# Optimization experiments

Measured on AMD Instinct MI355X. Metric: run time of the kernel, lower is better.

## Reference

```python
import jax, jax.numpy as jnp
import numpy as np

N_NODES = 100000
N_EDGES = 3200000  # avg degree 32
EPS = 1e-12


def setup_inputs() -> dict:
    key = jax.random.key(0)
    k1, k2, k3, k4, k5 = jax.random.split(key, 5)
    positions = jax.random.normal(k1, (N_NODES, 3), dtype=jnp.float32)
    node_feat = jnp.ones((N_NODES, 1), dtype=jnp.float32)  # dummy 1x0e data
    w0 = jax.random.normal(k2, (1,), dtype=jnp.float32)    # linear weight for 0e output
    w1 = jax.random.normal(k3, (3,), dtype=jnp.float32)    # linear weight for 1o output (elementwise)
    edge_src = jax.random.randint(k4, (N_EDGES,), 0, N_NODES, dtype=jnp.int32)
    edge_dst = jax.random.randint(k5, (N_EDGES,), 0, N_NODES, dtype=jnp.int32)
    return {"positions": positions, "node_feat": node_feat, "w0": w0, "w1": w1,
            "edge_src": edge_src, "edge_dst": edge_dst}


def reference(positions, node_feat, w0, w1, edge_src, edge_dst):
    n_nodes = positions.shape[0]
    # relative positions per edge: dest - src  [E,3]
    rel = positions[edge_dst] - positions[edge_src]
    # spherical harmonics lmax=1: Y0 = 1 (constant 0e), Y1 = unit direction (1o)
    norm = jnp.sqrt(jnp.sum(rel * rel, axis=-1, keepdims=True))
    sh1 = rel / jnp.maximum(norm, EPS)                      # [E,3]
    # gather dest-node scalar feature (code gathers dest_node_feat)
    s = node_feat[edge_dst]                                 # [E,1]
    # tensor product of 0e scalar with (0e + 1o): tp0 = s*1, tp1 = s*sh1
    # LinearLayer: elementwise multiply by per-irrep weight vectors
    out0 = w0 * s                                           # [E,1]
    out1 = w1 * (s * sh1)                                   # [E,3]
    edge_out = jnp.concatenate([out0, out1], axis=-1)       # [E,4]
    # scatter-mean aggregation over incoming edges per dest node
    sums = jax.ops.segment_sum(edge_out, edge_dst, num_segments=n_nodes)
    ones = jnp.ones((edge_out.shape[0], 1), dtype=edge_out.dtype)
    counts = jax.ops.segment_sum(ones, edge_dst, num_segments=n_nodes)
    return sums / jnp.maximum(counts, 1.0)                  # [N,4]
```

## Files before the change

### kernel.cpp

```cpp
#include <hip/hip_runtime.h>


#define EPS 1e-12f
#define FSCALE 128.0f
#define FBIAS 128
#define CHUNK_SHIFT 12
#define CHUNK 4096
#define NCHUNK_MAX 32
#define BLKA 512
#define TPA 4
#define NSTAGE (BLKA * TPA)
#define BLKB 512
#define SUBS 12
#define SHARDS 16

__global__ void repack_pos(const float* __restrict__ pos,
                           float4* __restrict__ pos4, int n_nodes) {
    int n = blockIdx.x * blockDim.x + threadIdx.x;
    if (n >= n_nodes) return;
    float4 p;
    p.x = pos[3 * n + 0];
    p.y = pos[3 * n + 1];
    p.z = pos[3 * n + 2];
    p.w = 0.f;
    pos4[n] = p;
}

__global__ __launch_bounds__(BLKA) void phaseA(
        const float4* __restrict__ pos4,
        const int* __restrict__ dst,
        const int* __restrict__ src,
        unsigned* __restrict__ gcnt,
        unsigned long long* __restrict__ recs,
        int n_edges, int capx, int n_chunk) {
    __shared__ unsigned long long stage[NSTAGE];
    __shared__ unsigned h[NCHUNK_MAX];
    __shared__ unsigned pref[NCHUNK_MAX + 1];
    __shared__ unsigned gbase[NCHUNK_MAX];
    int tid = threadIdx.x;
    int shard = (int)blockIdx.x & (SHARDS - 1);
    if (tid < n_chunk) h[tid] = 0;
    __syncthreads();

    long e0 = (long)blockIdx.x * NSTAGE;
    unsigned long long rec[TPA];
    int ch[TPA];
    unsigned rank[TPA];
    bool val[TPA];
#pragma unroll
    for (int t = 0; t < TPA; ++t) {
        long j = e0 + (long)t * BLKA + tid;
        val[t] = (j < n_edges);
        if (val[t]) {
            int d = dst[j];
            int s = src[j];
            float4 pd = pos4[d];
            float4 ps = pos4[s];
            float rx = pd.x - ps.x;
            float ry = pd.y - ps.y;
            float rz = pd.z - ps.z;
            float inv = 1.0f / fmaxf(sqrtf(rx * rx + ry * ry + rz * rz), EPS);
            unsigned fx = (unsigned)(FBIAS + (int)rintf(rx * inv * FSCALE));
            unsigned fy = (unsigned)(FBIAS + (int)rintf(ry * inv * FSCALE));
            unsigned fz = (unsigned)(FBIAS + (int)rintf(rz * inv * FSCALE));
            unsigned local = (unsigned)d & (CHUNK - 1);
            ch[t] = d >> CHUNK_SHIFT;
            rec[t] = ((unsigned long long)local << 27)
                   | ((unsigned long long)fx << 18)
                   | ((unsigned long long)fy << 9)
                   | (unsigned long long)fz;
            rank[t] = atomicAdd(&h[ch[t]], 1u);
        }
    }
    __syncthreads();
    if (tid == 0) {
        unsigned run = 0;
        for (int c = 0; c < n_chunk; ++c) { pref[c] = run; run += h[c]; }
        pref[n_chunk] = run;
    }
    if (tid < n_chunk)
        gbase[tid] = h[tid] ? atomicAdd(&gcnt[shard * NCHUNK_MAX + tid], h[tid]) : 0u;
    __syncthreads();
#pragma unroll
    for (int t = 0; t < TPA; ++t)
        if (val[t]) stage[pref[ch[t]] + rank[t]] = rec[t];
    __syncthreads();
    unsigned total = pref[n_chunk];
    for (unsigned i = tid; i < total; i += BLKA) {
        int lo = 0, hi = n_chunk - 1;
        while (lo < hi) {
            int mid = (lo + hi + 1) >> 1;
            if (pref[mid] <= i) lo = mid; else hi = mid - 1;
        }
        unsigned idx = gbase[lo] + (i - pref[lo]);
        if (idx < (unsigned)capx)
            recs[(size_t)(shard * n_chunk + lo) * (unsigned)capx + idx] = stage[i];
    }
}

__global__ __launch_bounds__(BLKB) void phaseB(
        const unsigned* __restrict__ gcnt,
        const unsigned long long* __restrict__ recs,
        unsigned long long* __restrict__ accR,
        int capx, int n_chunk, int padded) {
    __shared__ unsigned long long lds[CHUNK];
    int c   = (int)blockIdx.x % n_chunk;
    int sub = (int)blockIdx.x / n_chunk;

    for (int i = threadIdx.x; i < CHUNK; i += BLKB) lds[i] = 0ull;
    __syncthreads();

    for (int s16 = 0; s16 < SHARDS; ++s16) {
        unsigned cnt = gcnt[s16 * NCHUNK_MAX + c];
        if (cnt > (unsigned)capx) cnt = (unsigned)capx;
        const unsigned long long* bucket =
            recs + (size_t)(s16 * n_chunk + c) * (unsigned)capx;
        for (unsigned j = (unsigned)sub * BLKB + threadIdx.x; j < cnt;
             j += (unsigned)SUBS * BLKB) {
            unsigned long long r = bucket[j];
            unsigned local = (unsigned)(r >> 27);
            unsigned long long p = (((r >> 18) & 511ull) << 48)
                                 | (((r >>  9) & 511ull) << 32)
                                 | (((r      ) & 511ull) << 16)
                                 | 1ull;
            atomicAdd(&lds[local], p);
        }
    }
    __syncthreads();

    unsigned long long* row = accR + (size_t)sub * (unsigned)padded
                                   + (size_t)c * CHUNK;
    for (int i = threadIdx.x; i < CHUNK; i += BLKB) row[i] = lds[i];
}

__global__ void finalize_binned(const unsigned long long* __restrict__ accR,
                                const float* __restrict__ feat,
                                const float* __restrict__ w0,
                                const float* __restrict__ w1,
                                float* __restrict__ out,
                                int n_nodes, int padded) {
    int n = blockIdx.x * blockDim.x + threadIdx.x;
    if (n >= n_nodes) return;
    int Fx = 0, Fy = 0, Fz = 0, C = 0;
    for (int s = 0; s < SUBS; ++s) {
        unsigned long long v = accR[(size_t)s * (unsigned)padded + (unsigned)n];
        Fx += (int)(v >> 48);
        Fy += (int)((v >> 32) & 0xffffull);
        Fz += (int)((v >> 16) & 0xffffull);
        C  += (int)(v & 0xffffull);
    }
    float c = (float)C;
    float rd = 1.0f / fmaxf(c, 1.0f);
    float sx = (float)Fx * (1.0f / FSCALE) - c;
    float sy = (float)Fy * (1.0f / FSCALE) - c;
    float sz = (float)Fz * (1.0f / FSCALE) - c;
    float f = feat[n];
    float4 o;
    o.x = w0[0] * f * c * rd;
    o.y = w1[0] * f * sx * rd;
    o.z = w1[1] * f * sy * rd;
    o.w = w1[2] * f * sz * rd;
    ((float4*)out)[n] = o;
}

__global__ void edge_kernel_agent(const float* __restrict__ pos,
                                  const int* __restrict__ dst,
                                  const int* __restrict__ src,
                                  unsigned long long* __restrict__ acc,
                                  int n_edges, int n_nodes, int rmask) {
    int i = blockIdx.x * blockDim.x + threadIdx.x;
    if (i >= n_edges) return;
    int s = src[i];
    int d = dst[i];
    float rx = pos[3 * d + 0] - pos[3 * s + 0];
    float ry = pos[3 * d + 1] - pos[3 * s + 1];
    float rz = pos[3 * d + 2] - pos[3 * s + 2];
    float nrm = sqrtf(rx * rx + ry * ry + rz * rz);
    float inv = 1.0f / fmaxf(nrm, EPS);
    unsigned fx = (unsigned)(FBIAS + (int)rintf(rx * inv * FSCALE));
    unsigned fy = (unsigned)(FBIAS + (int)rintf(ry * inv * FSCALE));
    unsigned fz = (unsigned)(FBIAS + (int)rintf(rz * inv * FSCALE));
    unsigned long long p = ((unsigned long long)fx << 48)
                         | ((unsigned long long)fy << 32)
                         | ((unsigned long long)fz << 16) | 1ull;
    unsigned r = (unsigned)blockIdx.x & (unsigned)rmask;
    atomicAdd(acc + (size_t)r * (unsigned)n_nodes + (unsigned)d, p);
}

__global__ void finalize_flat(const unsigned long long* __restrict__ acc,
                              const float* __restrict__ feat,
                              const float* __restrict__ w0,
                              const float* __restrict__ w1,
                              float* __restrict__ out,
                              int n_nodes, int R) {
    int n = blockIdx.x * blockDim.x + threadIdx.x;
    if (n >= n_nodes) return;
    int Fx = 0, Fy = 0, Fz = 0, C = 0;
    for (int r = 0; r < R; ++r) {
        unsigned long long v = acc[(size_t)r * n_nodes + n];
        Fx += (int)(v >> 48);
        Fy += (int)((v >> 32) & 0xffffull);
        Fz += (int)((v >> 16) & 0xffffull);
        C  += (int)(v & 0xffffull);
    }
    float c = (float)C;
    float rd = 1.0f / fmaxf(c, 1.0f);
    float sx = (float)Fx * (1.0f / FSCALE) - c;
    float sy = (float)Fy * (1.0f / FSCALE) - c;
    float sz = (float)Fz * (1.0f / FSCALE) - c;
    float f = feat[n];
    float4 o;
    o.x = w0[0] * f * c * rd;
    o.y = w1[0] * f * sx * rd;
    o.z = w1[1] * f * sy * rd;
    o.w = w1[2] * f * sz * rd;
    ((float4*)out)[n] = o;
}

extern "C" void kernel_launch(void* const* d_in, const int* in_sizes, int n_in,
                              void* d_out, int out_size, void* d_ws, size_t ws_size,
                              hipStream_t stream) {
    const float* pos  = (const float*)d_in[0];
    const float* feat = (const float*)d_in[1];
    const float* w0   = (const float*)d_in[2];
    const float* w1   = (const float*)d_in[3];
    const int* esrc   = (const int*)d_in[4];
    const int* edst   = (const int*)d_in[5];
    int n_nodes = in_sizes[0] / 3;
    int n_edges = in_sizes[4];

    int n_chunk = (n_nodes + CHUNK - 1) >> CHUNK_SHIFT;
    int padded  = n_chunk * CHUNK;
    int capx = (int)((long)n_edges / ((long)SHARDS * n_chunk) + 4096);

    size_t off_pos4 = 0;
    size_t pos4_bytes = (size_t)padded * sizeof(float4);
    size_t off_gcnt = (pos4_bytes + 255) & ~(size_t)255;
    size_t gcnt_bytes = (size_t)SHARDS * NCHUNK_MAX * sizeof(unsigned);
    size_t off_recs = off_gcnt + ((gcnt_bytes + 255) & ~(size_t)255);
    size_t recs_bytes = (size_t)SHARDS * n_chunk * (unsigned)capx
                      * sizeof(unsigned long long);
    size_t off_accR = off_recs + ((recs_bytes + 255) & ~(size_t)255);
    size_t accR_bytes = (size_t)SUBS * (unsigned)padded * sizeof(unsigned long long);
    size_t need = off_accR + accR_bytes;

    int nb = 256;
    int ng = (n_nodes + nb - 1) / nb;

    if (n_chunk <= NCHUNK_MAX && ws_size >= need) {
        float4* pos4 = (float4*)((char*)d_ws + off_pos4);
        unsigned* gcnt = (unsigned*)((char*)d_ws + off_gcnt);
        unsigned long long* recs = (unsigned long long*)((char*)d_ws + off_recs);
        unsigned long long* accR = (unsigned long long*)((char*)d_ws + off_accR);

        hipMemsetAsync(gcnt, 0, gcnt_bytes, stream);
        repack_pos<<<ng, nb, 0, stream>>>(pos, pos4, n_nodes);

        int ga = (int)((n_edges + (long)NSTAGE - 1) / (long)NSTAGE);
        phaseA<<<ga, BLKA, 0, stream>>>(pos4, edst, esrc, gcnt, recs,
                                        n_edges, capx, n_chunk);
        phaseB<<<n_chunk * SUBS, BLKB, 0, stream>>>(gcnt, recs, accR,
                                                    capx, n_chunk, padded);
        finalize_binned<<<ng, nb, 0, stream>>>(accR, feat, w0, w1,
                                               (float*)d_out, n_nodes, padded);
    } else {
        int R = 4;
        while (R > 1 && (size_t)R * n_nodes * sizeof(unsigned long long) > ws_size) R >>= 1;
        unsigned long long* acc = (unsigned long long*)d_ws;
        hipMemsetAsync(acc, 0, (size_t)R * n_nodes * sizeof(unsigned long long), stream);
        int eb = 256;
        int eg = (n_edges + eb - 1) / eb;
        edge_kernel_agent<<<eg, eb, 0, stream>>>(pos, edst, esrc, acc,
                                                 n_edges, n_nodes, R - 1);
        finalize_flat<<<ng, nb, 0, stream>>>(acc, feat, w0, w1,
                                             (float*)d_out, n_nodes, R);
    }
}
```

Before: 133.2 us.

## Move geometry compute to phase B and bin compact 32-bit edge records

After: 119.8 us. 10.0% less time.

```diff
diff --git a/kernel.cpp b/kernel.cpp
--- a/kernel.cpp
+++ b/kernel.cpp
@@ -4,36 +4,38 @@
 #define EPS 1e-12f
 #define FSCALE 128.0f
 #define FBIAS 128
-#define CHUNK_SHIFT 12
-#define CHUNK 4096
-#define NCHUNK_MAX 32
+#define CHUNK_SHIFT 11
+#define CHUNK 2048
+#define NCHUNK_MAX 64
 #define BLKA 512
 #define TPA 4
 #define NSTAGE (BLKA * TPA)
 #define BLKB 512
-#define SUBS 12
 #define SHARDS 16
 
 __global__ void repack_pos(const float* __restrict__ pos,
-                           float4* __restrict__ pos4, int n_nodes) {
+                           float4* __restrict__ pos4,
+                           unsigned* __restrict__ gcnt,
+                           int n_nodes, int padded) {
     int n = blockIdx.x * blockDim.x + threadIdx.x;
-    if (n >= n_nodes) return;
-    float4 p;
-    p.x = pos[3 * n + 0];
-    p.y = pos[3 * n + 1];
-    p.z = pos[3 * n + 2];
-    p.w = 0.f;
+    if (n < SHARDS * NCHUNK_MAX) gcnt[n] = 0;
+    if (n >= padded) return;
+    float4 p = make_float4(0.f, 0.f, 0.f, 0.f);
+    if (n < n_nodes) {
+        p.x = pos[3 * n + 0];
+        p.y = pos[3 * n + 1];
+        p.z = pos[3 * n + 2];
+    }
     pos4[n] = p;
 }
 
 __global__ __launch_bounds__(BLKA) void phaseA(
-        const float4* __restrict__ pos4,
         const int* __restrict__ dst,
         const int* __restrict__ src,
         unsigned* __restrict__ gcnt,
-        unsigned long long* __restrict__ recs,
+        unsigned* __restrict__ recs,
         int n_edges, int capx, int n_chunk) {
-    __shared__ unsigned long long stage[NSTAGE];
+    __shared__ unsigned stage[NSTAGE];
     __shared__ unsigned h[NCHUNK_MAX];
     __shared__ unsigned pref[NCHUNK_MAX + 1];
     __shared__ unsigned gbase[NCHUNK_MAX];
@@ -43,7 +45,7 @@
     __syncthreads();
 
     long e0 = (long)blockIdx.x * NSTAGE;
-    unsigned long long rec[TPA];
+    unsigned rec[TPA];
     int ch[TPA];
     unsigned rank[TPA];
     bool val[TPA];
@@ -54,21 +56,8 @@
         if (val[t]) {
             int d = dst[j];
             int s = src[j];
-            float4 pd = pos4[d];
-            float4 ps = pos4[s];
-            float rx = pd.x - ps.x;
-            float ry = pd.y - ps.y;
-            float rz = pd.z - ps.z;
-            float inv = 1.0f / fmaxf(sqrtf(rx * rx + ry * ry + rz * rz), EPS);
-            unsigned fx = (unsigned)(FBIAS + (int)rintf(rx * inv * FSCALE));
-            unsigned fy = (unsigned)(FBIAS + (int)rintf(ry * inv * FSCALE));
-            unsigned fz = (unsigned)(FBIAS + (int)rintf(rz * inv * FSCALE));
-            unsigned local = (unsigned)d & (CHUNK - 1);
             ch[t] = d >> CHUNK_SHIFT;
-            rec[t] = ((unsigned long long)local << 27)
-                   | ((unsigned long long)fx << 18)
-                   | ((unsigned long long)fy << 9)
-                   | (unsigned long long)fz;
+            rec[t] = ((unsigned)(d & (CHUNK - 1)) << 17) | (unsigned)s;
             rank[t] = atomicAdd(&h[ch[t]], 1u);
         }
     }
@@ -100,37 +89,47 @@
 
 __global__ __launch_bounds__(BLKB) void phaseB(
         const unsigned* __restrict__ gcnt,
-        const unsigned long long* __restrict__ recs,
+        const unsigned* __restrict__ recs,
+        const float4* __restrict__ pos4,
         unsigned long long* __restrict__ accR,
         int capx, int n_chunk, int padded) {
-    __shared__ unsigned long long lds[CHUNK];
-    int c   = (int)blockIdx.x % n_chunk;
-    int sub = (int)blockIdx.x / n_chunk;
-
-    for (int i = threadIdx.x; i < CHUNK; i += BLKB) lds[i] = 0ull;
-    __syncthreads();
-
-    for (int s16 = 0; s16 < SHARDS; ++s16) {
-        unsigned cnt = gcnt[s16 * NCHUNK_MAX + c];
-        if (cnt > (unsigned)capx) cnt = (unsigned)capx;
-        const unsigned long long* bucket =
-            recs + (size_t)(s16 * n_chunk + c) * (unsigned)capx;
-        for (unsigned j = (unsigned)sub * BLKB + threadIdx.x; j < cnt;
-             j += (unsigned)SUBS * BLKB) {
-            unsigned long long r = bucket[j];
-            unsigned local = (unsigned)(r >> 27);
-            unsigned long long p = (((r >> 18) & 511ull) << 48)
-                                 | (((r >>  9) & 511ull) << 32)
-                                 | (((r      ) & 511ull) << 16)
-                                 | 1ull;
-            atomicAdd(&lds[local], p);
-        }
-    }
-    __syncthreads();
-
-    unsigned long long* row = accR + (size_t)sub * (unsigned)padded
-                                   + (size_t)c * CHUNK;
-    for (int i = threadIdx.x; i < CHUNK; i += BLKB) row[i] = lds[i];
+    __shared__ unsigned long long acc[CHUNK];
+    __shared__ float4 posw[CHUNK];
+    int c     = (int)blockIdx.x % n_chunk;
+    int shard = (int)blockIdx.x / n_chunk;
+    int base  = c << CHUNK_SHIFT;
+
+    for (int i = threadIdx.x; i < CHUNK; i += BLKB) {
+        acc[i] = 0ull;
+        posw[i] = pos4[base + i];
+    }
+    __syncthreads();
+
+    unsigned cnt = gcnt[shard * NCHUNK_MAX + c];
+    if (cnt > (unsigned)capx) cnt = (unsigned)capx;
+    const unsigned* bucket = recs + (size_t)(shard * n_chunk + c) * (unsigned)capx;
+    for (unsigned j = threadIdx.x; j < cnt; j += BLKB) {
+        unsigned r = bucket[j];
+        unsigned s = r & 0x1FFFFu;
+        unsigned local = r >> 17;
+        float4 ps = pos4[s];
+        float4 pd = posw[local];
+        float rx = pd.x - ps.x;
+        float ry = pd.y - ps.y;
+        float rz = pd.z - ps.z;
+        float inv = 1.0f / fmaxf(sqrtf(rx * rx + ry * ry + rz * rz), EPS);
+        unsigned fx = (unsigned)(FBIAS + (int)rintf(rx * inv * FSCALE));
+        unsigned fy = (unsigned)(FBIAS + (int)rintf(ry * inv * FSCALE));
+        unsigned fz = (unsigned)(FBIAS + (int)rintf(rz * inv * FSCALE));
+        unsigned long long p = ((unsigned long long)fx << 48)
+                             | ((unsigned long long)fy << 32)
+                             | ((unsigned long long)fz << 16) | 1ull;
+        atomicAdd(&acc[local], p);
+    }
+    __syncthreads();
+
+    unsigned long long* row = accR + (size_t)shard * (unsigned)padded + base;
+    for (int i = threadIdx.x; i < CHUNK; i += BLKB) row[i] = acc[i];
 }
 
 __global__ void finalize_binned(const unsigned long long* __restrict__ accR,
@@ -142,7 +141,7 @@
     int n = blockIdx.x * blockDim.x + threadIdx.x;
     if (n >= n_nodes) return;
     int Fx = 0, Fy = 0, Fz = 0, C = 0;
-    for (int s = 0; s < SUBS; ++s) {
+    for (int s = 0; s < SHARDS; ++s) {
         unsigned long long v = accR[(size_t)s * (unsigned)padded + (unsigned)n];
         Fx += (int)(v >> 48);
         Fy += (int)((v >> 32) & 0xffffull);
@@ -175,8 +174,7 @@
     float rx = pos[3 * d + 0] - pos[3 * s + 0];
     float ry = pos[3 * d + 1] - pos[3 * s + 1];
     float rz = pos[3 * d + 2] - pos[3 * s + 2];
-    float nrm = sqrtf(rx * rx + ry * ry + rz * rz);
-    float inv = 1.0f / fmaxf(nrm, EPS);
+    float inv = 1.0f / fmaxf(sqrtf(rx * rx + ry * ry + rz * rz), EPS);
     unsigned fx = (unsigned)(FBIAS + (int)rintf(rx * inv * FSCALE));
     unsigned fy = (unsigned)(FBIAS + (int)rintf(ry * inv * FSCALE));
     unsigned fz = (unsigned)(FBIAS + (int)rintf(rz * inv * FSCALE));
@@ -231,36 +229,35 @@
 
     int n_chunk = (n_nodes + CHUNK - 1) >> CHUNK_SHIFT;
     int padded  = n_chunk * CHUNK;
-    int capx = (int)((long)n_edges / ((long)SHARDS * n_chunk) + 4096);
+    int capx = (int)((long)n_edges / ((long)SHARDS * n_chunk) + 1024);
 
     size_t off_pos4 = 0;
     size_t pos4_bytes = (size_t)padded * sizeof(float4);
     size_t off_gcnt = (pos4_bytes + 255) & ~(size_t)255;
     size_t gcnt_bytes = (size_t)SHARDS * NCHUNK_MAX * sizeof(unsigned);
     size_t off_recs = off_gcnt + ((gcnt_bytes + 255) & ~(size_t)255);
-    size_t recs_bytes = (size_t)SHARDS * n_chunk * (unsigned)capx
-                      * sizeof(unsigned long long);
+    size_t recs_bytes = (size_t)SHARDS * n_chunk * (unsigned)capx * sizeof(unsigned);
     size_t off_accR = off_recs + ((recs_bytes + 255) & ~(size_t)255);
-    size_t accR_bytes = (size_t)SUBS * (unsigned)padded * sizeof(unsigned long long);
+    size_t accR_bytes = (size_t)SHARDS * (unsigned)padded * sizeof(unsigned long long);
     size_t need = off_accR + accR_bytes;
 
     int nb = 256;
     int ng = (n_nodes + nb - 1) / nb;
 
-    if (n_chunk <= NCHUNK_MAX && ws_size >= need) {
+    if (n_chunk <= NCHUNK_MAX && n_nodes <= (1 << 17) && ws_size >= need) {
         float4* pos4 = (float4*)((char*)d_ws + off_pos4);
         unsigned* gcnt = (unsigned*)((char*)d_ws + off_gcnt);
-        unsigned long long* recs = (unsigned long long*)((char*)d_ws + off_recs);
+        unsigned* recs = (unsigned*)((char*)d_ws + off_recs);
         unsigned long long* accR = (unsigned long long*)((char*)d_ws + off_accR);
 
-        hipMemsetAsync(gcnt, 0, gcnt_bytes, stream);
-        repack_pos<<<ng, nb, 0, stream>>>(pos, pos4, n_nodes);
+        int rg = (padded + nb - 1) / nb;
+        repack_pos<<<rg, nb, 0, stream>>>(pos, pos4, gcnt, n_nodes, padded);
 
         int ga = (int)((n_edges + (long)NSTAGE - 1) / (long)NSTAGE);
-        phaseA<<<ga, BLKA, 0, stream>>>(pos4, edst, esrc, gcnt, recs,
+        phaseA<<<ga, BLKA, 0, stream>>>(edst, esrc, gcnt, recs,
                                         n_edges, capx, n_chunk);
-        phaseB<<<n_chunk * SUBS, BLKB, 0, stream>>>(gcnt, recs, accR,
-                                                    capx, n_chunk, padded);
+        phaseB<<<n_chunk * SHARDS, BLKB, 0, stream>>>(gcnt, recs, pos4, accR,
+                                                      capx, n_chunk, padded);
         finalize_binned<<<ng, nb, 0, stream>>>(accR, feat, w0, w1,
                                                (float*)d_out, n_nodes, padded);
     } else {
```
